# Kernel tuning notes

Measured on AMD Instinct MI355X. Metric: run time of the kernel, lower is better.

Reference implementation:

```python
import jax, jax.numpy as jnp
import numpy as np

N = 100_000       # nodes
E = 1_600_000     # edges (avg degree 16)
F_IN = 10         # num_node_features
H = 128           # hidden_dim
L = 3             # num_layers
G = 256           # number of graphs in the batch
C = 25            # num_classes
BN_EPS = 1e-5


def setup_inputs() -> dict:
    key = jax.random.key(0)
    ks = jax.random.split(key, 10)
    s = 0.05
    x = jax.random.normal(ks[0], (N, F_IN), dtype=jnp.float32)
    edge_index = jax.random.randint(ks[1], (2, E), 0, N, dtype=jnp.int32)
    batch = jnp.sort(jax.random.randint(ks[2], (N,), 0, G, dtype=jnp.int32))
    return {
        "x": x,
        "edge_index": edge_index,
        "batch": batch,
        "Wp": jax.random.normal(ks[3], (F_IN, H), dtype=jnp.float32) * s,
        "bp": jnp.zeros((H,), jnp.float32),
        "Wc": jax.random.normal(ks[4], (L, H, H), dtype=jnp.float32) * s,
        "bc": jnp.zeros((L, H), jnp.float32),
        "bn_gamma": jnp.ones((L, H), jnp.float32),
        "bn_beta": jnp.zeros((L, H), jnp.float32),
        "bn_mean": jax.random.normal(ks[5], (L, H), dtype=jnp.float32) * 0.1,
        "bn_var": jax.random.uniform(ks[6], (L, H), minval=0.5, maxval=1.5, dtype=jnp.float32),
        "W1": jax.random.normal(ks[7], (2 * H, H), dtype=jnp.float32) * s,
        "b1": jnp.zeros((H,), jnp.float32),
        "W2": jax.random.normal(ks[8], (H, C), dtype=jnp.float32) * s,
        "b2": jnp.zeros((C,), jnp.float32),
    }


def reference(x, edge_index, batch, Wp, bp, Wc, bc, bn_gamma, bn_beta,
              bn_mean, bn_var, W1, b1, W2, b2):
    n = x.shape[0]
    # GCNConv: add self loops, symmetric degree normalization (eval semantics:
    # batchnorm uses running stats, dropout is identity).
    loop = jnp.arange(n, dtype=edge_index.dtype)
    rows = jnp.concatenate([edge_index[0], loop])  # target / aggregation index
    cols = jnp.concatenate([edge_index[1], loop])  # source / gather index
    deg = jax.ops.segment_sum(jnp.ones_like(rows, dtype=x.dtype), rows, num_segments=n)
    dinv = jax.lax.rsqrt(deg)  # deg >= 1 thanks to self loops
    norm = dinv[rows] * dinv[cols]  # [E+N]

    h = jax.nn.relu(x @ Wp + bp)
    for i in range(L):
        hw = h @ Wc[i]                                   # [N, H]
        msg = hw[cols] * norm[:, None]                   # gather + scale
        agg = jax.ops.segment_sum(msg, rows, num_segments=n) + bc[i]
        bn = (agg - bn_mean[i]) * jax.lax.rsqrt(bn_var[i] + BN_EPS) * bn_gamma[i] + bn_beta[i]
        h = jax.nn.relu(bn)

    counts = jax.ops.segment_sum(jnp.ones((n,), h.dtype), batch, num_segments=G)
    x_mean = jax.ops.segment_sum(h, batch, num_segments=G) / jnp.maximum(counts, 1.0)[:, None]
    x_max = jax.ops.segment_max(h, batch, num_segments=G)
    x_max = jnp.where(counts[:, None] > 0, x_max, 0.0)   # guard empty graphs
    g = jnp.concatenate([x_mean, x_max], axis=1)          # [G, 2H]
    return jax.nn.relu(g @ W1 + b1) @ W2 + b2             # [G, C]
```

## Files before the change

kernel.cpp:

```cpp
#include <hip/hip_runtime.h>

#define N_NODES   100000
#define N_EDGES   1600000
#define F_IN      10
#define HD        128
#define N_LAYERS  3
#define N_GRAPHS  256
#define N_CLASSES 25
#define BN_EPS    1e-5f
#define POOL_TILE 64
#define LDS_PITCH 152
#define CPITCH    136

#define NBUCK     196
#define SCAT_TILE 4096
#define BCAP      9216
#define BUCK_CAP  16384
#define PREPW_BLKS ((N_LAYERS*HD*HD)/256)
#define PROJ_BLKS 1024

#define AGG_ND    128
#define AGG_ECAP  4096

#define SLICE_U4  ((size_t)N_NODES*2)
#define SLICE_U1  ((size_t)N_NODES*8)

typedef __attribute__((ext_vector_type(8))) short bf8;
typedef __attribute__((ext_vector_type(4))) float f32x4;

static __device__ __forceinline__ unsigned short f2bf(float f){
    unsigned u = __float_as_uint(f);
    unsigned r = (u + 0x7fffu + ((u >> 16) & 1u)) >> 16;
    return (unsigned short)r;
}
static __device__ __forceinline__ float bflo(unsigned u){ return __uint_as_float(u << 16); }
static __device__ __forceinline__ float bfhi(unsigned u){ return __uint_as_float(u & 0xffff0000u); }
static __device__ __forceinline__ unsigned packbf(float a, float b){
    return (unsigned)f2bf(a) | ((unsigned)f2bf(b) << 16);
}

__global__ __launch_bounds__(256) void k_scatter(const int* __restrict__ rows,
        const int* __restrict__ cols, int* __restrict__ gcur,
        unsigned* __restrict__ ebuf, int e, int nsb,
        const float* __restrict__ Wc, unsigned short* __restrict__ WT,
        const float* __restrict__ x, const float* __restrict__ Wp,
        const float* __restrict__ bp, unsigned* __restrict__ hbf, int n){
    __shared__ int lbase[NBUCK];
    __shared__ int lcur[NBUCK];
    __shared__ int gbase[NBUCK];
    __shared__ int sbuf[256];
    __shared__ unsigned sedge[SCAT_TILE];
    __shared__ unsigned char sbuck[SCAT_TILE];
    __shared__ float sW[F_IN*HD];
    __shared__ float sb[HD];
    int t = threadIdx.x;

    if (blockIdx.x >= nsb){
        int bid2 = blockIdx.x - nsb;
        if (bid2 < PREPW_BLKS){
            int i = bid2*256 + t;
            int l = i >> 14;
            int r = (i >> 7) & 127;
            int c = i & 127;
            WT[(l << 14) + c*HD + r] = f2bf(Wc[i]);
            return;
        }
        int bid = bid2 - PREPW_BLKS;
        for (int q = t; q < F_IN*HD; q += 256) sW[q] = Wp[q];
        if (t < HD) sb[t] = bp[t];
        __syncthreads();
        int j  = t & 63;
        int ln = t >> 6;
        size_t sbase = (size_t)(j >> 3)*SLICE_U1 + (j & 7);
        for (int n0 = bid*4 + ln; n0 < n; n0 += PROJ_BLKS*4){
            float a0 = sb[2*j], a1 = sb[2*j+1];
            #pragma unroll
            for (int k = 0; k < F_IN; k++){
                float xv = x[(size_t)n0*F_IN + k];
                a0 += xv * sW[k*HD + 2*j];
                a1 += xv * sW[k*HD + 2*j+1];
            }
            hbf[sbase + (size_t)n0*8] = packbf(fmaxf(a0, 0.f), fmaxf(a1, 0.f));
        }
        return;
    }

    int i0 = blockIdx.x*SCAT_TILE + t;
    int r[16], c[16];
    if (t < NBUCK) lcur[t] = 0;
    __syncthreads();
    #pragma unroll
    for (int k = 0; k < 16; k++){
        int i = i0 + k*256;
        if (i < e){
            r[k] = rows[i]; c[k] = cols[i];
            atomicAdd(&lcur[r[k] >> 9], 1);
        } else r[k] = -1;
    }
    __syncthreads();
    int myc = (t < NBUCK) ? lcur[t] : 0;
    sbuf[t] = myc;
    __syncthreads();
    for (int d = 1; d < 256; d <<= 1){
        int tv = (t >= d) ? sbuf[t-d] : 0;
        __syncthreads();
        sbuf[t] += tv;
        __syncthreads();
    }
    if (t < NBUCK){
        lbase[t] = sbuf[t] - myc;
        lcur[t]  = sbuf[t] - myc;
        if (myc > 0) gbase[t] = t*BCAP + atomicAdd(&gcur[t], myc);
    }
    __syncthreads();
    #pragma unroll
    for (int k = 0; k < 16; k++){
        if (r[k] >= 0){
            int bk = r[k] >> 9;
            int off = atomicAdd(&lcur[bk], 1);
            sedge[off] = ((unsigned)(r[k] & 511) << 17) | (unsigned)c[k];
            sbuck[off] = (unsigned char)bk;
        }
    }
    __syncthreads();
    int tot = sbuf[255];
    for (int i = t; i < tot; i += 256){
        int bk = sbuck[i];
        ebuf[gbase[bk] + (i - lbase[bk])] = sedge[i];
    }
}

__global__ __launch_bounds__(512) void k_build(const unsigned* __restrict__ ebuf,
        const int* __restrict__ gcur, int* __restrict__ rowptr,
        float* __restrict__ dinv, int* __restrict__ colidx, int n, int etot){
    __shared__ int hist[512];
    __shared__ int cur[512];
    __shared__ int colstage[BUCK_CAP];
    __shared__ int sscan[256];
    int t = threadIdx.x;
    int gval = (t < NBUCK) ? gcur[t] : 0;
    if (t < 256) sscan[t] = gval;
    __syncthreads();
    for (int d = 1; d < 256; d <<= 1){
        int tv = (t < 256 && t >= d) ? sscan[t-d] : 0;
        __syncthreads();
        if (t < 256) sscan[t] += tv;
        __syncthreads();
    }
    int b = blockIdx.x;
    int cnt = gcur[b];
    int s   = sscan[b] - cnt;
    int sp  = b*BCAP;
    int row0 = b << 9;
    int nrows = min(512, n - row0);
    if (b == 0 && t == 0) rowptr[n] = etot;
    hist[t] = 0;
    __syncthreads();
    for (int i = t; i < cnt; i += 512)
        atomicAdd(&hist[ebuf[sp + i] >> 17], 1);
    __syncthreads();
    int myc = hist[t];
    cur[t] = myc;
    __syncthreads();
    for (int d = 1; d < 512; d <<= 1){
        int tv = (t >= d) ? cur[t-d] : 0;
        __syncthreads();
        cur[t] += tv;
        __syncthreads();
    }
    int excl = cur[t] - myc;
    if (t < nrows){
        rowptr[row0 + t] = s + excl;
        dinv[row0 + t] = rsqrtf((float)(myc + 1));
    }
    cur[t] = excl;
    __syncthreads();
    for (int i = t; i < cnt; i += 512){
        unsigned v = ebuf[sp + i];
        int off = atomicAdd(&cur[v >> 17], 1);
        colstage[off] = (int)(v & 0x1ffffu);
    }
    __syncthreads();
    for (int i = t; i < cnt; i += 512)
        colidx[s + i] = colstage[i];
}

__global__ __launch_bounds__(512) void k_gemm(const uint4* __restrict__ h4,
        const unsigned short* __restrict__ WT, const float* __restrict__ dinv,
        uint4* __restrict__ hw, int n){
    extern __shared__ char smem[];
    unsigned short* As = (unsigned short*)smem;
    unsigned short* Bs = As + 128*LDS_PITCH;
    int tid = threadIdx.x;
    int row0 = blockIdx.x * 128;

    const uint4* w4 = (const uint4*)WT;
    #pragma unroll
    for (int q = tid; q < 1024; q += 512){
        int r = q & 127, sc = q >> 7;
        int grow = row0 + r;
        uint4 v0 = make_uint4(0u,0u,0u,0u), v1 = v0;
        if (grow < n){
            size_t bidx = (size_t)sc*SLICE_U4 + (size_t)grow*2;
            v0 = h4[bidx]; v1 = h4[bidx + 1];
        }
        *(uint4*)&As[r*LDS_PITCH + sc*16]     = v0;
        *(uint4*)&As[r*LDS_PITCH + sc*16 + 8] = v1;
    }
    #pragma unroll
    for (int q = tid; q < 2048; q += 512){
        int r = q >> 4, c = q & 15;
        *(uint4*)&Bs[r*LDS_PITCH + c*8] = w4[r*16 + c];
    }
    __syncthreads();

    int w = tid >> 6, lane = tid & 63;
    int l15 = lane & 15, quad = lane >> 4;
    f32x4 acc[8];
    #pragma unroll
    for (int ct = 0; ct < 8; ct++) acc[ct] = (f32x4){0.f,0.f,0.f,0.f};

    int arow = w*16 + l15;
    #pragma unroll
    for (int kc = 0; kc < 4; kc++){
        int ko = kc*32 + quad*8;
        bf8 a = *(const bf8*)&As[arow*LDS_PITCH + ko];
        #pragma unroll
        for (int ct = 0; ct < 8; ct++){
            bf8 b = *(const bf8*)&Bs[(ct*16 + l15)*LDS_PITCH + ko];
            acc[ct] = __builtin_amdgcn_mfma_f32_16x16x32_bf16(a, b, acc[ct], 0, 0, 0);
        }
    }
    __syncthreads();

    unsigned short* CS = As;
    #pragma unroll
    for (int reg = 0; reg < 4; reg++){
        int rloc = w*16 + quad*4 + reg;
        int grow = row0 + rloc;
        float dv = (grow < n) ? dinv[grow] : 0.f;
        #pragma unroll
        for (int ct = 0; ct < 8; ct++)
            CS[rloc*CPITCH + ct*16 + l15] = f2bf(acc[ct][reg] * dv);
    }
    __syncthreads();

    #pragma unroll
    for (int q = tid; q < 1024; q += 512){
        int r = q & 127, sc = q >> 7;
        int grow = row0 + r;
        if (grow < n){
            size_t bidx = (size_t)sc*SLICE_U4 + (size_t)grow*2;
            hw[bidx]     = *(const uint4*)&CS[r*CPITCH + sc*16];
            hw[bidx + 1] = *(const uint4*)&CS[r*CPITCH + sc*16 + 8];
        }
    }
}

__global__ __launch_bounds__(256) void k_agg(const uint4* __restrict__ hw4,
        const int* __restrict__ rowptr, const int* __restrict__ colidx,
        const float* __restrict__ dinv, const float* __restrict__ bc,
        const float* __restrict__ bmean, const float* __restrict__ bvar,
        const float* __restrict__ bgamma, const float* __restrict__ bbeta,
        uint4* __restrict__ houtb, int n){
    __shared__ int scol[AGG_ECAP];
    __shared__ int srp[AGG_ND + 1];
    int tid = threadIdx.x;
    int slice = blockIdx.x & 7;
    int chunk = blockIdx.x >> 3;
    int n0 = chunk * AGG_ND;
    int nloc = min(AGG_ND, n - n0);

    for (int i = tid; i <= nloc; i += 256) srp[i] = rowptr[n0 + i];
    __syncthreads();
    int ebase = srp[0];
    int ecnt  = srp[nloc] - ebase;
    bool inl = (ecnt <= AGG_ECAP);
    if (inl){
        for (int i = tid; i < ecnt; i += 256) scol[i] = colidx[ebase + i];
    }
    __syncthreads();
    const int* col = inl ? (const int*)scol : (colidx + ebase);

    int nd = tid >> 1, hf = tid & 1;
    bool valid = nd < nloc;
    int node = n0 + (valid ? nd : 0);
    const uint4* base = hw4 + (size_t)slice*SLICE_U4;

    float a[8], b[8];
    uint4 self = base[(size_t)node*2 + hf];
    a[0] = bflo(self.x); a[1] = bfhi(self.x);
    a[2] = bflo(self.y); a[3] = bfhi(self.y);
    a[4] = bflo(self.z); a[5] = bfhi(self.z);
    a[6] = bflo(self.w); a[7] = bfhi(self.w);
    #pragma unroll
    for (int j = 0; j < 8; j++) b[j] = 0.f;

    int s = valid ? (srp[nd]   - ebase) : 0;
    int e = valid ? (srp[nd+1] - ebase) : 0;
    int t = s;

    #define ACC(dst, v) { dst[0]+=bflo(v.x); dst[1]+=bfhi(v.x); \
                          dst[2]+=bflo(v.y); dst[3]+=bfhi(v.y); \
                          dst[4]+=bflo(v.z); dst[5]+=bfhi(v.z); \
                          dst[6]+=bflo(v.w); dst[7]+=bfhi(v.w); }

    for (; t + 8 <= e; t += 8){
        int c0 = col[t],   c1 = col[t+1];
        int c2 = col[t+2], c3 = col[t+3];
        int c4 = col[t+4], c5 = col[t+5];
        int c6 = col[t+6], c7 = col[t+7];
        uint4 v0 = base[(size_t)c0*2 + hf];
        uint4 v1 = base[(size_t)c1*2 + hf];
        uint4 v2 = base[(size_t)c2*2 + hf];
        uint4 v3 = base[(size_t)c3*2 + hf];
        uint4 v4 = base[(size_t)c4*2 + hf];
        uint4 v5 = base[(size_t)c5*2 + hf];
        uint4 v6 = base[(size_t)c6*2 + hf];
        uint4 v7 = base[(size_t)c7*2 + hf];
        ACC(a, v0); ACC(b, v1); ACC(a, v2); ACC(b, v3);
        ACC(a, v4); ACC(b, v5); ACC(a, v6); ACC(b, v7);
    }
    for (; t + 4 <= e; t += 4){
        int c0 = col[t],   c1 = col[t+1];
        int c2 = col[t+2], c3 = col[t+3];
        uint4 v0 = base[(size_t)c0*2 + hf];
        uint4 v1 = base[(size_t)c1*2 + hf];
        uint4 v2 = base[(size_t)c2*2 + hf];
        uint4 v3 = base[(size_t)c3*2 + hf];
        ACC(a, v0); ACC(b, v1); ACC(a, v2); ACC(b, v3);
    }
    for (; t < e; t++){
        uint4 v = base[(size_t)col[t]*2 + hf];
        ACC(a, v);
    }
    #undef ACC
    #pragma unroll
    for (int j = 0; j < 8; j++) a[j] += b[j];

    if (!valid) return;
    float dv = dinv[node];
    int f4 = slice*4 + hf*2;
    float cb[8], cm[8], cv[8], cg[8], ct[8];
    *(float4*)&cb[0] = ((const float4*)bc)[f4];     *(float4*)&cb[4] = ((const float4*)bc)[f4+1];
    *(float4*)&cm[0] = ((const float4*)bmean)[f4];  *(float4*)&cm[4] = ((const float4*)bmean)[f4+1];
    *(float4*)&cv[0] = ((const float4*)bvar)[f4];   *(float4*)&cv[4] = ((const float4*)bvar)[f4+1];
    *(float4*)&cg[0] = ((const float4*)bgamma)[f4]; *(float4*)&cg[4] = ((const float4*)bgamma)[f4+1];
    *(float4*)&ct[0] = ((const float4*)bbeta)[f4];  *(float4*)&ct[4] = ((const float4*)bbeta)[f4+1];
    float r[8];
    #pragma unroll
    for (int j = 0; j < 8; j++){
        float rx = (a[j]*dv + cb[j] - cm[j]) * rsqrtf(cv[j] + BN_EPS) * cg[j] + ct[j];
        r[j] = fmaxf(rx, 0.f);
    }
    uint4 o;
    o.x = packbf(r[0], r[1]);
    o.y = packbf(r[2], r[3]);
    o.z = packbf(r[4], r[5]);
    o.w = packbf(r[6], r[7]);
    houtb[(size_t)slice*SLICE_U4 + (size_t)node*2 + hf] = o;
}

__global__ void k_pool(const unsigned* __restrict__ hb, const int* __restrict__ batch,
        float* __restrict__ gsum, int* __restrict__ gmax, int n){
    int q = threadIdx.x;
    int start = blockIdx.x * POOL_TILE;
    int end = min(start + POOL_TILE, n);
    if (start >= end) return;
    size_t sbase = (size_t)(q >> 3)*SLICE_U1 + (q & 7);
    int cur = batch[start];
    float s0 = 0.f, s1 = 0.f, m0 = 0.f, m1 = 0.f;
    for (int i = start; i < end; i++){
        int b = batch[i];
        unsigned v = hb[sbase + (size_t)i*8];
        float v0 = bflo(v), v1 = bfhi(v);
        if (b != cur){
            atomicAdd(&gsum[cur*HD + 2*q],     s0);
            atomicAdd(&gsum[cur*HD + 2*q + 1], s1);
            atomicMax(&gmax[cur*HD + 2*q],     __float_as_int(m0));
            atomicMax(&gmax[cur*HD + 2*q + 1], __float_as_int(m1));
            s0 = s1 = m0 = m1 = 0.f; cur = b;
        }
        s0 += v0; s1 += v1;
        m0 = fmaxf(m0, v0); m1 = fmaxf(m1, v1);
    }
    atomicAdd(&gsum[cur*HD + 2*q],     s0);
    atomicAdd(&gsum[cur*HD + 2*q + 1], s1);
    atomicMax(&gmax[cur*HD + 2*q],     __float_as_int(m0));
    atomicMax(&gmax[cur*HD + 2*q + 1], __float_as_int(m1));
}

__global__ void k_head(const float* __restrict__ gsum, const int* __restrict__ gmax,
        const int* __restrict__ batch, const float* __restrict__ W1,
        const float* __restrict__ b1, const float* __restrict__ W2,
        const float* __restrict__ b2, float* __restrict__ out, int n){
    __shared__ float gv[2*HD];
    __shared__ float hid[HD];
    __shared__ int bound[2];
    int g = blockIdx.x, j = threadIdx.x;
    if (j < 2){
        int target = g + j;
        int lo = 0, hi = n;
        while (lo < hi){ int mid = (lo + hi) >> 1; if (batch[mid] < target) lo = mid + 1; else hi = mid; }
        bound[j] = lo;
    }
    __syncthreads();
    float denom = (float)max(bound[1] - bound[0], 1);
    gv[j]    = gsum[g*HD+j] / denom;
    gv[HD+j] = __int_as_float(gmax[g*HD+j]);
    __syncthreads();
    float acc = b1[j];
    #pragma unroll 8
    for (int k = 0; k < 2*HD; k++) acc += gv[k]*W1[k*HD + j];
    hid[j] = fmaxf(acc, 0.f);
    __syncthreads();
    if (j < N_CLASSES){
        float o = b2[j];
        #pragma unroll 4
        for (int k = 0; k < HD; k++) o += hid[k]*W2[k*N_CLASSES + j];
        out[g*N_CLASSES + j] = o;
    }
}

extern "C" void kernel_launch(void* const* d_in, const int* in_sizes, int n_in,
                              void* d_out, int out_size, void* d_ws, size_t ws_size,
                              hipStream_t stream){
    const float* x   = (const float*)d_in[0];
    const int*  eidx = (const int*)d_in[1];
    const int* batch = (const int*)d_in[2];
    const float* Wp  = (const float*)d_in[3];
    const float* bp  = (const float*)d_in[4];
    const float* Wc  = (const float*)d_in[5];
    const float* bc  = (const float*)d_in[6];
    const float* bng = (const float*)d_in[7];
    const float* bnb = (const float*)d_in[8];
    const float* bnm = (const float*)d_in[9];
    const float* bnv = (const float*)d_in[10];
    const float* W1  = (const float*)d_in[11];
    const float* b1  = (const float*)d_in[12];
    const float* W2  = (const float*)d_in[13];
    const float* b2  = (const float*)d_in[14];
    float* out = (float*)d_out;

    char* ws = (char*)d_ws;
    size_t off = 0;
    unsigned short* h_bf  = (unsigned short*)(ws + off); off += (size_t)N_NODES*HD*2;
    unsigned short* hw_bf = (unsigned short*)(ws + off); off += (size_t)N_NODES*HD*2;
    unsigned short* WT = (unsigned short*)(ws + off); off += (size_t)N_LAYERS*HD*HD*2;
    float* dinv   = (float*)(ws + off); off += (size_t)N_NODES*4;
    int*   rowptr = (int*)  (ws + off); off += (size_t)(N_NODES+16)*4;
    int*   colidx = (int*)  (ws + off); off += (size_t)N_EDGES*4;
    unsigned* ebuf= (unsigned*)(ws + off); off += (size_t)NBUCK*BCAP*4;
    int*   gcur   = (int*)  (ws + off); off += 1024;
    float* gsum   = (float*)(ws + off); off += (size_t)N_GRAPHS*HD*4;
    int*   gmax   = (int*)  (ws + off); off += (size_t)N_GRAPHS*HD*4;

    const int* rows = eidx;
    const int* cols = eidx + N_EDGES;

    hipMemsetAsync(gcur, 0, 1024 + (size_t)(N_GRAPHS*HD*2)*4, stream);

    int nsb = (N_EDGES + SCAT_TILE - 1)/SCAT_TILE;
    k_scatter<<<nsb + PREPW_BLKS + PROJ_BLKS, 256, 0, stream>>>(rows, cols, gcur, ebuf,
        N_EDGES, nsb, Wc, WT, x, Wp, bp, (unsigned*)h_bf, N_NODES);
    k_build  <<<NBUCK, 512, 0, stream>>>(ebuf, gcur, rowptr, dinv, colidx, N_NODES, N_EDGES);

    int ntiles = (N_NODES + 127)/128;
    int aggblk = ((N_NODES + AGG_ND - 1)/AGG_ND) * 8;
    size_t shmem = (size_t)(2*128*LDS_PITCH)*2;
    for (int l = 0; l < N_LAYERS; l++){
        k_gemm<<<ntiles, 512, shmem, stream>>>((const uint4*)h_bf, WT + (size_t)l*HD*HD, dinv,
            (uint4*)hw_bf, N_NODES);
        k_agg<<<aggblk, 256, 0, stream>>>((const uint4*)hw_bf, rowptr, colidx, dinv,
            bc + l*HD, bnm + l*HD, bnv + l*HD, bng + l*HD, bnb + l*HD,
            (uint4*)h_bf, N_NODES);
    }

    k_pool<<<(N_NODES+POOL_TILE-1)/POOL_TILE, 64, 0, stream>>>((const unsigned*)h_bf, batch, gsum, gmax, N_NODES);
    k_head<<<N_GRAPHS, 128, 0, stream>>>(gsum, gmax, batch, W1, b1, W2, b2, out, N_NODES);
}
```

Baseline: 443.6 us.

## Spread each node's edges across 8 lanes in GCN aggregation with shuffle reduction

The aggregation kernel now assigns 16 lanes per node (8 edge-parallel lanes times 2 halves) and loops over node groups, rather than one lane pair walking a node's whole edge list. Partial sums are combined with xor shuffles, and the BN constants are loaded and rsqrt'd once per thread. This is meant to cut per-lane serial latency and degree-driven imbalance within a wave, but each node now takes several sequential group iterations and shuffle overhead, and there is less memory-level parallelism per lane.

```diff
diff --git a/kernel.cpp b/kernel.cpp
--- a/kernel.cpp
+++ b/kernel.cpp
@@ -282,83 +282,87 @@
     __syncthreads();
     const int* col = inl ? (const int*)scol : (colidx + ebase);
 
-    int nd = tid >> 1, hf = tid & 1;
-    bool valid = nd < nloc;
-    int node = n0 + (valid ? nd : 0);
     const uint4* base = hw4 + (size_t)slice*SLICE_U4;
-
-    float a[8], b[8];
-    uint4 self = base[(size_t)node*2 + hf];
-    a[0] = bflo(self.x); a[1] = bfhi(self.x);
-    a[2] = bflo(self.y); a[3] = bfhi(self.y);
-    a[4] = bflo(self.z); a[5] = bfhi(self.z);
-    a[6] = bflo(self.w); a[7] = bfhi(self.w);
-    #pragma unroll
-    for (int j = 0; j < 8; j++) b[j] = 0.f;
-
-    int s = valid ? (srp[nd]   - ebase) : 0;
-    int e = valid ? (srp[nd+1] - ebase) : 0;
-    int t = s;
+    int wid  = tid >> 6;
+    int lane = tid & 63;
+    int grp  = lane >> 4;
+    int ep   = (lane >> 1) & 7;
+    int hf   = lane & 1;
+
+    int f4 = slice*4 + hf*2;
+    float cb[8], cm[8], rs[8], cg[8], cbe[8];
+    {
+        float cv[8];
+        *(float4*)&cb[0]  = ((const float4*)bc)[f4];     *(float4*)&cb[4]  = ((const float4*)bc)[f4+1];
+        *(float4*)&cm[0]  = ((const float4*)bmean)[f4];  *(float4*)&cm[4]  = ((const float4*)bmean)[f4+1];
+        *(float4*)&cv[0]  = ((const float4*)bvar)[f4];   *(float4*)&cv[4]  = ((const float4*)bvar)[f4+1];
+        *(float4*)&cg[0]  = ((const float4*)bgamma)[f4]; *(float4*)&cg[4]  = ((const float4*)bgamma)[f4+1];
+        *(float4*)&cbe[0] = ((const float4*)bbeta)[f4];  *(float4*)&cbe[4] = ((const float4*)bbeta)[f4+1];
+        #pragma unroll
+        for (int j = 0; j < 8; j++) rs[j] = rsqrtf(cv[j] + BN_EPS);
+    }
 
     #define ACC(dst, v) { dst[0]+=bflo(v.x); dst[1]+=bfhi(v.x); \
                           dst[2]+=bflo(v.y); dst[3]+=bfhi(v.y); \
                           dst[4]+=bflo(v.z); dst[5]+=bfhi(v.z); \
                           dst[6]+=bflo(v.w); dst[7]+=bfhi(v.w); }
 
-    for (; t + 8 <= e; t += 8){
-        int c0 = col[t],   c1 = col[t+1];
-        int c2 = col[t+2], c3 = col[t+3];
-        int c4 = col[t+4], c5 = col[t+5];
-        int c6 = col[t+6], c7 = col[t+7];
-        uint4 v0 = base[(size_t)c0*2 + hf];
-        uint4 v1 = base[(size_t)c1*2 + hf];
-        uint4 v2 = base[(size_t)c2*2 + hf];
-        uint4 v3 = base[(size_t)c3*2 + hf];
-        uint4 v4 = base[(size_t)c4*2 + hf];
-        uint4 v5 = base[(size_t)c5*2 + hf];
-        uint4 v6 = base[(size_t)c6*2 + hf];
-        uint4 v7 = base[(size_t)c7*2 + hf];
-        ACC(a, v0); ACC(b, v1); ACC(a, v2); ACC(b, v3);
-        ACC(a, v4); ACC(b, v5); ACC(a, v6); ACC(b, v7);
-    }
-    for (; t + 4 <= e; t += 4){
-        int c0 = col[t],   c1 = col[t+1];
-        int c2 = col[t+2], c3 = col[t+3];
-        uint4 v0 = base[(size_t)c0*2 + hf];
-        uint4 v1 = base[(size_t)c1*2 + hf];
-        uint4 v2 = base[(size_t)c2*2 + hf];
-        uint4 v3 = base[(size_t)c3*2 + hf];
-        ACC(a, v0); ACC(b, v1); ACC(a, v2); ACC(b, v3);
-    }
-    for (; t < e; t++){
-        uint4 v = base[(size_t)col[t]*2 + hf];
-        ACC(a, v);
+    #pragma unroll 1
+    for (int g = 0; g < AGG_ND/16; g++){
+        int nd = g*16 + wid*4 + grp;
+        bool valid = nd < nloc;
+        int node = n0 + (valid ? nd : 0);
+        int s   = valid ? (srp[nd]   - ebase) : 0;
+        int deg = valid ? (srp[nd+1] - ebase) - s : 0;
+
+        float a[8];
+        #pragma unroll
+        for (int j = 0; j < 8; j++) a[j] = 0.f;
+        if (valid && ep == 0){
+            uint4 self = base[(size_t)node*2 + hf];
+            a[0] = bflo(self.x); a[1] = bfhi(self.x);
+            a[2] = bflo(self.y); a[3] = bfhi(self.y);
+            a[4] = bflo(self.z); a[5] = bfhi(self.z);
+            a[6] = bflo(self.w); a[7] = bfhi(self.w);
+        }
+
+        for (int t = 0; t < deg; t += 16){
+            int i0 = t + ep;
+            int i1 = t + 8 + ep;
+            if (i0 < deg){
+                uint4 v = base[(size_t)col[s + i0]*2 + hf];
+                ACC(a, v);
+            }
+            if (i1 < deg){
+                uint4 v = base[(size_t)col[s + i1]*2 + hf];
+                ACC(a, v);
+            }
+        }
+
+        #pragma unroll
+        for (int j = 0; j < 8; j++){
+            a[j] += __shfl_xor(a[j], 2, 64);
+            a[j] += __shfl_xor(a[j], 4, 64);
+            a[j] += __shfl_xor(a[j], 8, 64);
+        }
+
+        if (valid && ep == 0){
+            float dv = dinv[node];
+            float r[8];
+            #pragma unroll
+            for (int j = 0; j < 8; j++){
+                float rx = (a[j]*dv + cb[j] - cm[j]) * rs[j] * cg[j] + cbe[j];
+                r[j] = fmaxf(rx, 0.f);
+            }
+            uint4 o;
+            o.x = packbf(r[0], r[1]);
+            o.y = packbf(r[2], r[3]);
+            o.z = packbf(r[4], r[5]);
+            o.w = packbf(r[6], r[7]);
+            houtb[(size_t)slice*SLICE_U4 + (size_t)node*2 + hf] = o;
+        }
     }
     #undef ACC
-    #pragma unroll
-    for (int j = 0; j < 8; j++) a[j] += b[j];
-
-    if (!valid) return;
-    float dv = dinv[node];
-    int f4 = slice*4 + hf*2;
-    float cb[8], cm[8], cv[8], cg[8], ct[8];
-    *(float4*)&cb[0] = ((const float4*)bc)[f4];     *(float4*)&cb[4] = ((const float4*)bc)[f4+1];
-    *(float4*)&cm[0] = ((const float4*)bmean)[f4];  *(float4*)&cm[4] = ((const float4*)bmean)[f4+1];
-    *(float4*)&cv[0] = ((const float4*)bvar)[f4];   *(float4*)&cv[4] = ((const float4*)bvar)[f4+1];
-    *(float4*)&cg[0] = ((const float4*)bgamma)[f4]; *(float4*)&cg[4] = ((const float4*)bgamma)[f4+1];
-    *(float4*)&ct[0] = ((const float4*)bbeta)[f4];  *(float4*)&ct[4] = ((const float4*)bbeta)[f4+1];
-    float r[8];
-    #pragma unroll
-    for (int j = 0; j < 8; j++){
-        float rx = (a[j]*dv + cb[j] - cm[j]) * rsqrtf(cv[j] + BN_EPS) * cg[j] + ct[j];
-        r[j] = fmaxf(rx, 0.f);
-    }
-    uint4 o;
-    o.x = packbf(r[0], r[1]);
-    o.y = packbf(r[2], r[3]);
-    o.z = packbf(r[4], r[5]);
-    o.w = packbf(r[6], r[7]);
-    houtb[(size_t)slice*SLICE_U4 + (size_t)node*2 + hf] = o;
 }
 
 __global__ void k_pool(const unsigned* __restrict__ hb, const int* __restrict__ batch,
```

After: 519.6 us. +17.1%, slower.

## Sort nodes by degree for aggregation and prefetch edge column indices

Applied to the files above, without the earlier changes.

Adds a histogram, scan and permutation pass that groups nodes by in-degree, and makes the aggregation kernel walk nodes in that order. Nodes in the same wavefront then have similar edge counts, which is meant to cut idle lanes caused by uneven loop trip counts. The aggregation loop also loads the next batch of eight column indices while the current gathers are in flight, and the 4-wide and scalar tail loops become one predicated unrolled tail. In exchange, column indices are no longer staged in LDS, and rowptr, colidx and output accesses become scattered because neighbouring threads now handle non-adjacent nodes. Three small extra kernel launches are added as well.

```diff
diff --git a/kernel.cpp b/kernel.cpp
--- a/kernel.cpp
+++ b/kernel.cpp
@@ -18,9 +18,6 @@
 #define BUCK_CAP  16384
 #define PREPW_BLKS ((N_LAYERS*HD*HD)/256)
 #define PROJ_BLKS 1024
-
-#define AGG_ND    128
-#define AGG_ECAP  4096
 
 #define SLICE_U4  ((size_t)N_NODES*2)
 #define SLICE_U1  ((size_t)N_NODES*8)
@@ -185,6 +182,43 @@
         colidx[s + i] = colstage[i];
 }
 
+__global__ __launch_bounds__(256) void k_hist(const int* __restrict__ rowptr,
+        int* __restrict__ bins, int n){
+    __shared__ int lb[256];
+    int t = threadIdx.x;
+    lb[t] = 0;
+    __syncthreads();
+    int i = blockIdx.x*256 + t;
+    if (i < n){
+        int d = rowptr[i+1] - rowptr[i];
+        atomicAdd(&lb[min(d, 255)], 1);
+    }
+    __syncthreads();
+    if (lb[t]) atomicAdd(&bins[t], lb[t]);
+}
+__global__ void k_scan(const int* __restrict__ bins, int* __restrict__ cursors){
+    __shared__ int sb[256];
+    int t = threadIdx.x;
+    sb[t] = bins[t];
+    __syncthreads();
+    for (int d = 1; d < 256; d <<= 1){
+        int v = (t >= d) ? sb[t-d] : 0;
+        __syncthreads();
+        sb[t] += v;
+        __syncthreads();
+    }
+    cursors[t] = sb[t] - bins[t];
+}
+__global__ __launch_bounds__(256) void k_permout(const int* __restrict__ rowptr,
+        int* __restrict__ cursors, int* __restrict__ perm, int n){
+    int i = blockIdx.x*256 + threadIdx.x;
+    if (i < n){
+        int d = rowptr[i+1] - rowptr[i];
+        int pos = atomicAdd(&cursors[min(d, 255)], 1);
+        perm[pos] = i;
+    }
+}
+
 __global__ __launch_bounds__(512) void k_gemm(const uint4* __restrict__ h4,
         const unsigned short* __restrict__ WT, const float* __restrict__ dinv,
         uint4* __restrict__ hw, int n){
@@ -259,32 +293,17 @@
 
 __global__ __launch_bounds__(256) void k_agg(const uint4* __restrict__ hw4,
         const int* __restrict__ rowptr, const int* __restrict__ colidx,
-        const float* __restrict__ dinv, const float* __restrict__ bc,
-        const float* __restrict__ bmean, const float* __restrict__ bvar,
-        const float* __restrict__ bgamma, const float* __restrict__ bbeta,
-        uint4* __restrict__ houtb, int n){
-    __shared__ int scol[AGG_ECAP];
-    __shared__ int srp[AGG_ND + 1];
+        const int* __restrict__ perm, const float* __restrict__ dinv,
+        const float* __restrict__ bc, const float* __restrict__ bmean,
+        const float* __restrict__ bvar, const float* __restrict__ bgamma,
+        const float* __restrict__ bbeta, uint4* __restrict__ houtb, int n){
     int tid = threadIdx.x;
     int slice = blockIdx.x & 7;
     int chunk = blockIdx.x >> 3;
-    int n0 = chunk * AGG_ND;
-    int nloc = min(AGG_ND, n - n0);
-
-    for (int i = tid; i <= nloc; i += 256) srp[i] = rowptr[n0 + i];
-    __syncthreads();
-    int ebase = srp[0];
-    int ecnt  = srp[nloc] - ebase;
-    bool inl = (ecnt <= AGG_ECAP);
-    if (inl){
-        for (int i = tid; i < ecnt; i += 256) scol[i] = colidx[ebase + i];
-    }
-    __syncthreads();
-    const int* col = inl ? (const int*)scol : (colidx + ebase);
-
-    int nd = tid >> 1, hf = tid & 1;
-    bool valid = nd < nloc;
-    int node = n0 + (valid ? nd : 0);
+    int idx = chunk*128 + (tid >> 1);
+    int hf  = tid & 1;
+    bool valid = idx < n;
+    int node = valid ? perm[idx] : 0;
     const uint4* base = hw4 + (size_t)slice*SLICE_U4;
 
     float a[8], b[8];
@@ -296,8 +315,8 @@
     #pragma unroll
     for (int j = 0; j < 8; j++) b[j] = 0.f;
 
-    int s = valid ? (srp[nd]   - ebase) : 0;
-    int e = valid ? (srp[nd+1] - ebase) : 0;
+    int s = rowptr[node];
+    int e = valid ? rowptr[node+1] : s;
     int t = s;
 
     #define ACC(dst, v) { dst[0]+=bflo(v.x); dst[1]+=bfhi(v.x); \
@@ -305,11 +324,14 @@
                           dst[4]+=bflo(v.z); dst[5]+=bfhi(v.z); \
                           dst[6]+=bflo(v.w); dst[7]+=bfhi(v.w); }
 
-    for (; t + 8 <= e; t += 8){
-        int c0 = col[t],   c1 = col[t+1];
-        int c2 = col[t+2], c3 = col[t+3];
-        int c4 = col[t+4], c5 = col[t+5];
-        int c6 = col[t+6], c7 = col[t+7];
+    int c0=0,c1=0,c2=0,c3=0,c4=0,c5=0,c6=0,c7=0;
+    if (t + 8 <= e){
+        c0 = colidx[t];   c1 = colidx[t+1];
+        c2 = colidx[t+2]; c3 = colidx[t+3];
+        c4 = colidx[t+4]; c5 = colidx[t+5];
+        c6 = colidx[t+6]; c7 = colidx[t+7];
+    }
+    while (t + 8 <= e){
         uint4 v0 = base[(size_t)c0*2 + hf];
         uint4 v1 = base[(size_t)c1*2 + hf];
         uint4 v2 = base[(size_t)c2*2 + hf];
@@ -318,22 +340,34 @@
         uint4 v5 = base[(size_t)c5*2 + hf];
         uint4 v6 = base[(size_t)c6*2 + hf];
         uint4 v7 = base[(size_t)c7*2 + hf];
+        int tn = t + 8;
+        if (tn + 8 <= e){
+            c0 = colidx[tn];   c1 = colidx[tn+1];
+            c2 = colidx[tn+2]; c3 = colidx[tn+3];
+            c4 = colidx[tn+4]; c5 = colidx[tn+5];
+            c6 = colidx[tn+6]; c7 = colidx[tn+7];
+        }
         ACC(a, v0); ACC(b, v1); ACC(a, v2); ACC(b, v3);
         ACC(a, v4); ACC(b, v5); ACC(a, v6); ACC(b, v7);
-    }
-    for (; t + 4 <= e; t += 4){
-        int c0 = col[t],   c1 = col[t+1];
-        int c2 = col[t+2], c3 = col[t+3];
-        uint4 v0 = base[(size_t)c0*2 + hf];
-        uint4 v1 = base[(size_t)c1*2 + hf];
-        uint4 v2 = base[(size_t)c2*2 + hf];
-        uint4 v3 = base[(size_t)c3*2 + hf];
-        ACC(a, v0); ACC(b, v1); ACC(a, v2); ACC(b, v3);
-    }
-    for (; t < e; t++){
-        uint4 v = base[(size_t)col[t]*2 + hf];
-        ACC(a, v);
-    }
+        t = tn;
+    }
+
+    int rem = e - t;
+    uint4 w0, w1, w2, w3, w4, w5, w6;
+    if (rem > 0) w0 = base[(size_t)colidx[t]*2 + hf];
+    if (rem > 1) w1 = base[(size_t)colidx[t+1]*2 + hf];
+    if (rem > 2) w2 = base[(size_t)colidx[t+2]*2 + hf];
+    if (rem > 3) w3 = base[(size_t)colidx[t+3]*2 + hf];
+    if (rem > 4) w4 = base[(size_t)colidx[t+4]*2 + hf];
+    if (rem > 5) w5 = base[(size_t)colidx[t+5]*2 + hf];
+    if (rem > 6) w6 = base[(size_t)colidx[t+6]*2 + hf];
+    if (rem > 0) ACC(a, w0);
+    if (rem > 1) ACC(b, w1);
+    if (rem > 2) ACC(a, w2);
+    if (rem > 3) ACC(b, w3);
+    if (rem > 4) ACC(a, w4);
+    if (rem > 5) ACC(b, w5);
+    if (rem > 6) ACC(a, w6);
     #undef ACC
     #pragma unroll
     for (int j = 0; j < 8; j++) a[j] += b[j];
@@ -452,26 +486,34 @@
     int*   colidx = (int*)  (ws + off); off += (size_t)N_EDGES*4;
     unsigned* ebuf= (unsigned*)(ws + off); off += (size_t)NBUCK*BCAP*4;
     int*   gcur   = (int*)  (ws + off); off += 1024;
+    int*   bins   = (int*)  (ws + off); off += 1024;
     float* gsum   = (float*)(ws + off); off += (size_t)N_GRAPHS*HD*4;
     int*   gmax   = (int*)  (ws + off); off += (size_t)N_GRAPHS*HD*4;
+    int*   cursors= (int*)  (ws + off); off += 1024;
+    int*   perm   = (int*)  (ws + off); off += (size_t)N_NODES*4;
 
     const int* rows = eidx;
     const int* cols = eidx + N_EDGES;
 
-    hipMemsetAsync(gcur, 0, 1024 + (size_t)(N_GRAPHS*HD*2)*4, stream);
+    hipMemsetAsync(gcur, 0, 2048 + (size_t)(N_GRAPHS*HD*2)*4, stream);
 
     int nsb = (N_EDGES + SCAT_TILE - 1)/SCAT_TILE;
     k_scatter<<<nsb + PREPW_BLKS + PROJ_BLKS, 256, 0, stream>>>(rows, cols, gcur, ebuf,
         N_EDGES, nsb, Wc, WT, x, Wp, bp, (unsigned*)h_bf, N_NODES);
     k_build  <<<NBUCK, 512, 0, stream>>>(ebuf, gcur, rowptr, dinv, colidx, N_NODES, N_EDGES);
 
+    int nb = (N_NODES + 255)/256;
+    k_hist   <<<nb, 256, 0, stream>>>(rowptr, bins, N_NODES);
+    k_scan   <<<1, 256, 0, stream>>>(bins, cursors);
+    k_permout<<<nb, 256, 0, stream>>>(rowptr, cursors, perm, N_NODES);
+
     int ntiles = (N_NODES + 127)/128;
-    int aggblk = ((N_NODES + AGG_ND - 1)/AGG_ND) * 8;
+    int aggblk = ntiles * 8;
     size_t shmem = (size_t)(2*128*LDS_PITCH)*2;
     for (int l = 0; l < N_LAYERS; l++){
         k_gemm<<<ntiles, 512, shmem, stream>>>((const uint4*)h_bf, WT + (size_t)l*HD*HD, dinv,
             (uint4*)hw_bf, N_NODES);
-        k_agg<<<aggblk, 256, 0, stream>>>((const uint4*)hw_bf, rowptr, colidx, dinv,
+        k_agg<<<aggblk, 256, 0, stream>>>((const uint4*)hw_bf, rowptr, colidx, perm, dinv,
             bc + l*HD, bnm + l*HD, bnv + l*HD, bng + l*HD, bnb + l*HD,
             (uint4*)h_bf, N_NODES);
     }
```

After: 821.6 us. 85.2% more time.
